# Optimization experiments

Measured on AMD Instinct MI355X. Metric: run time of the kernel, lower is better.

The kernel has to match this reference:

```python
import jax, jax.numpy as jnp
import numpy as np

TOPK = 8
MAX_DISP = 2.0
_EPS = 1e-6
_BIG = 1e9


def _projection(coords, P):
    # coords: [N,3,L,M] 3D points, P: [N,3,4] camera projection matrix
    X = jnp.einsum('nij,njlm->nilm', P[:, :, :3], coords) + P[:, :, 3][:, :, None, None]
    z = jnp.maximum(X[:, 2], _EPS)          # [N,L,M] depth, clamped
    x2d = X[:, :2] / z[:, None]             # [N,2,L,M] perspective divide
    return x2d, z


def _nms(x2d, topk, max_disp):
    # Greedy per-pixel NMS over candidate axis M.
    # x2d: [P, M, 2] -> selected candidate indices [P, topk].
    # Candidates are scanned in order; a candidate is kept if its 2D location is
    # farther than max_disp (L2) from every previously kept candidate, until topk kept.
    Pn, M, _ = x2d.shape
    slots = jnp.arange(topk)
    thr2 = max_disp * max_disp

    def step(carry, xm):
        sel_c, sel_i, cnt = carry           # [P,topk,2], [P,topk] int32, [P] int32
        m, coord = xm                       # scalar, [P,2]
        d2 = jnp.sum((sel_c - coord[:, None, :]) ** 2, axis=-1)  # [P,topk]
        suppressed = jnp.any(d2 <= thr2, axis=1)
        keep = (~suppressed) & (cnt < topk)
        onehot = (slots[None, :] == cnt[:, None]) & keep[:, None]  # write slot
        sel_c = jnp.where(onehot[..., None], coord[:, None, :], sel_c)
        sel_i = jnp.where(onehot, m.astype(jnp.int32), sel_i)
        return (sel_c, sel_i, cnt + keep.astype(jnp.int32)), None

    init = (jnp.full((Pn, topk, 2), _BIG, x2d.dtype),
            jnp.zeros((Pn, topk), jnp.int32),
            jnp.zeros((Pn,), jnp.int32))
    (_, sel_i, _), _ = jax.lax.scan(step, init, (jnp.arange(M), jnp.swapaxes(x2d, 0, 1)))
    return sel_i


def setup_inputs() -> dict:
    key = jax.random.key(0)
    k1, k2 = jax.random.split(key)
    N, M, H, W = 16, 32, 120, 160
    coords = jax.random.normal(k1, (N, M, 3, H, W), jnp.float32)
    # pixel-scale x/y spread and positive depth so projection is well-behaved
    coords = coords.at[:, :, :2].multiply(50.0).at[:, :, 2].add(5.0)
    P0 = jnp.concatenate([jnp.eye(3, dtype=jnp.float32), jnp.zeros((3, 1), jnp.float32)], axis=1)
    anchor_P = P0[None] + 0.01 * jax.random.normal(k2, (N, 3, 4), jnp.float32)
    return {"coords_grid": coords, "anchor_P": anchor_P}


def reference(coords_grid, anchor_P):
    N, M, _, H, W = coords_grid.shape
    c = jnp.transpose(coords_grid, (0, 2, 3, 4, 1)).reshape(N, 3, H * W, M)
    x2d, _ = _projection(c, anchor_P)                               # [N,2,HW,M]
    x2d_grid = jnp.transpose(x2d, (0, 2, 3, 1)).reshape(N, H, W, M, 2)
    idxs = _nms(x2d_grid.reshape(N * H * W, M, 2), TOPK, MAX_DISP)  # [NHW,topk]
    return idxs.reshape(N, H, W, TOPK).astype(jnp.int32)
```

## Files before the change

### kernel.cpp

```cpp
#include <hip/hip_runtime.h>

#define TOPK 8
#define MM 32

__global__ __launch_bounds__(256) void nms_proj_kernel(
    const float* __restrict__ coords, const float* __restrict__ P,
    int* __restrict__ out, int N, int HW)
{
    const float THR2 = 4.0f;
    const float EPSV = 1e-6f;
    const float BIGV = 1e9f;

    int pix = blockIdx.x * blockDim.x + threadIdx.x;
    int total = N * HW;
    if (pix >= total) return;

    int n = pix / HW;
    int hw = pix - n * HW;

    const float* Pp = P + n * 12;
    float p00 = Pp[0], p01 = Pp[1], p02 = Pp[2],  p03 = Pp[3];
    float p10 = Pp[4], p11 = Pp[5], p12 = Pp[6],  p13 = Pp[7];
    float p20 = Pp[8], p21 = Pp[9], p22 = Pp[10], p23 = Pp[11];

    const float* base = coords + (size_t)n * (MM * 3) * HW + hw;

    float kx[TOPK], ky[TOPK];
    int sel[TOPK];
#pragma unroll
    for (int s = 0; s < TOPK; ++s) { kx[s] = BIGV; ky[s] = BIGV; sel[s] = 0; }
    int cnt = 0;

    for (int m = 0; m < MM; ++m) {
        if (__all(cnt >= TOPK)) break;

        const float* cm = base + (size_t)m * (3 * HW);
        float X0 = cm[0];
        float X1 = cm[HW];
        float X2 = cm[2 * HW];

        float xc = p00 * X0 + p01 * X1 + p02 * X2 + p03;
        float yc = p10 * X0 + p11 * X1 + p12 * X2 + p13;
        float zc = p20 * X0 + p21 * X1 + p22 * X2 + p23;
        float z  = fmaxf(zc, EPSV);
        float x  = xc / z;
        float y  = yc / z;

        bool sup = false;
#pragma unroll
        for (int s = 0; s < TOPK; ++s) {
            float dx = kx[s] - x;
            float dy = ky[s] - y;
            sup = sup || (dx * dx + dy * dy <= THR2);
        }
        bool keep = (!sup) && (cnt < TOPK);
        if (keep) {
#pragma unroll
            for (int s = 0; s < TOPK; ++s) {
                if (s == cnt) { kx[s] = x; ky[s] = y; sel[s] = m; }
            }
            cnt++;
        }
    }

    int4* o = reinterpret_cast<int4*>(out + (size_t)pix * TOPK);
    o[0] = make_int4(sel[0], sel[1], sel[2], sel[3]);
    o[1] = make_int4(sel[4], sel[5], sel[6], sel[7]);
}

extern "C" void kernel_launch(void* const* d_in, const int* in_sizes, int n_in,
                              void* d_out, int out_size, void* d_ws, size_t ws_size,
                              hipStream_t stream) {
    const float* coords = (const float*)d_in[0];
    const float* P      = (const float*)d_in[1];
    int* out            = (int*)d_out;

    int N  = in_sizes[1] / 12;
    int HW = in_sizes[0] / (N * MM * 3);
    int total = N * HW;

    int block = 256;
    int grid = (total + block - 1) / block;
    nms_proj_kernel<<<grid, block, 0, stream>>>(coords, P, out, N, HW);
}
```

Before: 158.4 us.

## Prefetch coordinate candidates in groups of four with register double-buffering

Measured after the change: 161.7 us. +2.1%, slower.

```diff
diff --git a/kernel.cpp b/kernel.cpp
--- a/kernel.cpp
+++ b/kernel.cpp
@@ -2,6 +2,7 @@
 
 #define TOPK 8
 #define MM 32
+#define MG 4
 
 __global__ __launch_bounds__(256) void nms_proj_kernel(
     const float* __restrict__ coords, const float* __restrict__ P,
@@ -24,6 +25,7 @@
     float p20 = Pp[8], p21 = Pp[9], p22 = Pp[10], p23 = Pp[11];
 
     const float* base = coords + (size_t)n * (MM * 3) * HW + hw;
+    const size_t mstride = (size_t)3 * HW;
 
     float kx[TOPK], ky[TOPK];
     int sel[TOPK];
@@ -31,36 +33,57 @@
     for (int s = 0; s < TOPK; ++s) { kx[s] = BIGV; ky[s] = BIGV; sel[s] = 0; }
     int cnt = 0;
 
-    for (int m = 0; m < MM; ++m) {
+    float X0[MG], X1[MG], X2[MG];
+#pragma unroll
+    for (int g = 0; g < MG; ++g) {
+        const float* cm = base + (size_t)g * mstride;
+        X0[g] = cm[0]; X1[g] = cm[HW]; X2[g] = cm[2 * HW];
+    }
+
+    for (int mb = 0; mb < MM; mb += MG) {
         if (__all(cnt >= TOPK)) break;
 
-        const float* cm = base + (size_t)m * (3 * HW);
-        float X0 = cm[0];
-        float X1 = cm[HW];
-        float X2 = cm[2 * HW];
+        float nX0[MG], nX1[MG], nX2[MG];
+        if (mb + MG < MM) {
+#pragma unroll
+            for (int g = 0; g < MG; ++g) {
+                const float* cm = base + (size_t)(mb + MG + g) * mstride;
+                nX0[g] = cm[0]; nX1[g] = cm[HW]; nX2[g] = cm[2 * HW];
+            }
+        } else {
+#pragma unroll
+            for (int g = 0; g < MG; ++g) { nX0[g] = 0.f; nX1[g] = 0.f; nX2[g] = 0.f; }
+        }
 
-        float xc = p00 * X0 + p01 * X1 + p02 * X2 + p03;
-        float yc = p10 * X0 + p11 * X1 + p12 * X2 + p13;
-        float zc = p20 * X0 + p21 * X1 + p22 * X2 + p23;
-        float z  = fmaxf(zc, EPSV);
-        float x  = xc / z;
-        float y  = yc / z;
+#pragma unroll
+        for (int g = 0; g < MG; ++g) {
+            int m = mb + g;
+            float xc = p00 * X0[g] + p01 * X1[g] + p02 * X2[g] + p03;
+            float yc = p10 * X0[g] + p11 * X1[g] + p12 * X2[g] + p13;
+            float zc = p20 * X0[g] + p21 * X1[g] + p22 * X2[g] + p23;
+            float z  = fmaxf(zc, EPSV);
+            float x  = xc / z;
+            float y  = yc / z;
 
-        bool sup = false;
-#pragma unroll
-        for (int s = 0; s < TOPK; ++s) {
-            float dx = kx[s] - x;
-            float dy = ky[s] - y;
-            sup = sup || (dx * dx + dy * dy <= THR2);
-        }
-        bool keep = (!sup) && (cnt < TOPK);
-        if (keep) {
+            bool sup = false;
 #pragma unroll
             for (int s = 0; s < TOPK; ++s) {
-                if (s == cnt) { kx[s] = x; ky[s] = y; sel[s] = m; }
+                float dx = kx[s] - x;
+                float dy = ky[s] - y;
+                sup = sup || (dx * dx + dy * dy <= THR2);
             }
-            cnt++;
+            bool keep = (!sup) && (cnt < TOPK);
+            if (keep) {
+#pragma unroll
+                for (int s = 0; s < TOPK; ++s) {
+                    if (s == cnt) { kx[s] = x; ky[s] = y; sel[s] = m; }
+                }
+                cnt++;
+            }
         }
+
+#pragma unroll
+        for (int g = 0; g < MG; ++g) { X0[g] = nX0[g]; X1[g] = nX1[g]; X2[g] = nX2[g]; }
     }
 
     int4* o = reinterpret_cast<int4*>(out + (size_t)pix * TOPK);
```
